# Kernel tuning notes

Hardware: AMD Instinct MI355X
Metric: run time of the kernel (lower is better)

The kernel has to match this reference:

```python
import jax, jax.numpy as jnp
import numpy as np

N = 20000      # num_nodes
E = 320000     # num_edges
T = 24         # seq_len
SD = 16        # static_dim
DD = 8         # dynamic_dim
HID = 128      # hidden_dim
HEADS = 4
DPH = HID // HEADS  # per-head dim (GATConv out_channels = hidden_dim // heads)
L = 3          # num_gnn_layers
LN_EPS = 1e-5


def setup_inputs() -> dict:
    key = jax.random.key(0)
    ks = jax.random.split(key, 16)
    f = lambda i, shape, s=0.1: jax.random.normal(ks[i], shape, jnp.float32) * s
    return {
        "x_static": f(0, (N, SD), 1.0),
        "x_dynamic": f(1, (T, N, DD), 1.0),
        "edge_index": jax.random.randint(ks[2], (2, E), 0, N),
        "proj_W": f(3, (SD + DD, HID)),
        "proj_b": jnp.zeros((HID,), jnp.float32),
        "gat_W": f(4, (L, HID, HID)),
        "att_src": f(5, (L, HEADS, DPH)),
        "att_dst": f(6, (L, HEADS, DPH)),
        "gat_b": jnp.zeros((L, HID), jnp.float32),
        "ln_g": jnp.ones((L, HID), jnp.float32),
        "ln_b": jnp.zeros((L, HID), jnp.float32),
        "lstm_Wih0": f(7, (4 * HID, HID)),
        "lstm_Whh0": f(8, (4 * HID, HID)),
        "lstm_bih0": jnp.zeros((4 * HID,), jnp.float32),
        "lstm_bhh0": jnp.zeros((4 * HID,), jnp.float32),
        "lstm_Wih1": f(9, (4 * HID, HID)),
        "lstm_Whh1": f(10, (4 * HID, HID)),
        "lstm_bih1": jnp.zeros((4 * HID,), jnp.float32),
        "lstm_bhh1": jnp.zeros((4 * HID,), jnp.float32),
        "out_W1": f(11, (HID, HID // 2)),
        "out_b1": jnp.zeros((HID // 2,), jnp.float32),
        "out_W2": f(12, (HID // 2, 1)),
        "out_b2": jnp.zeros((1,), jnp.float32),
    }


def _gat_layer(h, src, dst, W, a_s, a_d, b, g, beta):
    """PyG GATConv (self-loops already in src/dst) + residual + LayerNorm + ReLU."""
    Nn = h.shape[0]
    xp = (h @ W).reshape(Nn, HEADS, DPH)                # [N, H, D]
    a_src = (xp * a_s).sum(-1)                          # [N, H]
    a_dst = (xp * a_d).sum(-1)                          # [N, H]
    e = jax.nn.leaky_relu(a_src[src] + a_dst[dst], 0.2)  # [E', H]
    m = jax.ops.segment_max(e, dst, num_segments=Nn)
    ex = jnp.exp(e - m[dst])
    denom = jax.ops.segment_sum(ex, dst, num_segments=Nn)
    alpha = ex / (denom[dst] + 1e-16)                   # segment softmax over in-edges
    msg = xp[src] * alpha[:, :, None]                   # [E', H, D]
    out = jax.ops.segment_sum(msg, dst, num_segments=Nn).reshape(Nn, HID) + b
    out = out + h                                       # residual (dims match)
    mu = out.mean(-1, keepdims=True)
    var = ((out - mu) ** 2).mean(-1, keepdims=True)
    out = g * (out - mu) * jax.lax.rsqrt(var + LN_EPS) + beta
    return jax.nn.relu(out)


def _lstm_cell(x, h, c, Wih, Whh, bih, bhh):
    z = x @ Wih.T + h @ Whh.T + bih + bhh
    i, f, gg, o = jnp.split(z, 4, axis=-1)              # torch gate order i,f,g,o
    c = jax.nn.sigmoid(f) * c + jax.nn.sigmoid(i) * jnp.tanh(gg)
    h = jax.nn.sigmoid(o) * jnp.tanh(c)
    return h, c


def reference(x_static, x_dynamic, edge_index, proj_W, proj_b, gat_W, att_src,
              att_dst, gat_b, ln_g, ln_b, lstm_Wih0, lstm_Whh0, lstm_bih0,
              lstm_bhh0, lstm_Wih1, lstm_Whh1, lstm_bih1, lstm_bhh1,
              out_W1, out_b1, out_W2, out_b2):
    Nn = x_static.shape[0]
    loop = jnp.arange(Nn)
    src = jnp.concatenate([edge_index[0], loop])        # GATConv add_self_loops=True
    dst = jnp.concatenate([edge_index[1], loop])

    @jax.checkpoint
    def timestep(xd_t):
        h = jnp.concatenate([x_static, xd_t], axis=-1) @ proj_W + proj_b
        for l in range(L):
            h = _gat_layer(h, src, dst, gat_W[l], att_src[l], att_dst[l],
                           gat_b[l], ln_g[l], ln_b[l])
        return h

    h_seq = jax.lax.map(timestep, x_dynamic)            # [T, N, HID]

    def step(carry, x_t):
        h0, c0, h1, c1 = carry
        h0, c0 = _lstm_cell(x_t, h0, c0, lstm_Wih0, lstm_Whh0, lstm_bih0, lstm_bhh0)
        h1, c1 = _lstm_cell(h0, h1, c1, lstm_Wih1, lstm_Whh1, lstm_bih1, lstm_bhh1)
        return (h0, c0, h1, c1), None

    z = jnp.zeros((Nn, HID), x_static.dtype)
    (_, _, h1, _), _ = jax.lax.scan(step, (z, z, z, z), h_seq)
    pred = jax.nn.relu(h1 @ out_W1 + out_b1) @ out_W2 + out_b2
    return pred[:, 0]
```

## Files before the change

### kernel.cpp

```cpp
#include <hip/hip_runtime.h>
#include <hip/hip_bf16.h>
#include <math.h>

#define NN   20000
#define NE   320000
#define TT   24
#define SDIM 16
#define DDIM 8
#define HID  128
#define HEADS 4
#define DPH  32
#define NL   3
#define TC   4

typedef unsigned short u16;
typedef unsigned int   u32;
typedef __attribute__((ext_vector_type(8))) short  short8;
typedef __attribute__((ext_vector_type(4))) float  floatx4;

__device__ __forceinline__ u16 f2bf(float x) {
  u32 u = __float_as_uint(x);
  return (u16)((u + 0x7fff + ((u >> 16) & 1)) >> 16);
}
__device__ __forceinline__ float bf2f(u16 b) {
  return __uint_as_float(((u32)b) << 16);
}

__global__ void k_count(const int* __restrict__ dst, int* __restrict__ cnt) {
  int e = blockIdx.x * 256 + threadIdx.x;
  if (e < NE) atomicAdd(&cnt[dst[e]], 1);
}

__global__ __launch_bounds__(1024) void k_scan(const int* __restrict__ cnt,
    int* __restrict__ rowptr, int* __restrict__ cursor) {
  __shared__ int sh[1024];
  int tid = threadIdx.x;
  const int CH = 20;
  int base = tid * CH;
  int local[CH];
  int s = 0;
  #pragma unroll
  for (int i = 0; i < CH; i++) {
    int idx = base + i;
    int v = (idx < NN) ? cnt[idx] : 0;
    local[i] = s;
    s += v;
  }
  sh[tid] = s;
  __syncthreads();
  for (int off = 1; off < 1024; off <<= 1) {
    int tv = (tid >= off) ? sh[tid - off] : 0;
    __syncthreads();
    sh[tid] += tv;
    __syncthreads();
  }
  int pre = (tid > 0) ? sh[tid - 1] : 0;
  #pragma unroll
  for (int i = 0; i < CH; i++) {
    int idx = base + i;
    if (idx < NN) { int e = pre + local[i]; rowptr[idx] = e; cursor[idx] = e; }
  }
  if (tid == 1023) rowptr[NN] = sh[1023];
}

__global__ void k_fill(const int* __restrict__ src, const int* __restrict__ dst,
    int* __restrict__ cursor, int* __restrict__ col) {
  int e = blockIdx.x * 256 + threadIdx.x;
  if (e < NE) {
    int pos = atomicAdd(&cursor[dst[e]], 1);
    col[pos] = src[e];
  }
}

__global__ void k_prepw_lstm(const float* __restrict__ Wih, const float* __restrict__ Whh,
    u16* __restrict__ Bt) {
  int idx = blockIdx.x * 256 + threadIdx.x;
  if (idx < 512 * 256) {
    int jp = idx >> 8, k = idx & 255;
    int c = jp >> 2, g = jp & 3;
    int j = g * 128 + c;
    float v = (k < 128) ? Wih[(size_t)j * 128 + k] : Whh[(size_t)j * 128 + (k - 128)];
    Bt[idx] = f2bf(v);
  }
}
__global__ void k_prepb(const float* __restrict__ bih0, const float* __restrict__ bhh0,
    const float* __restrict__ bih1, const float* __restrict__ bhh1,
    float* __restrict__ bs01) {
  int t = threadIdx.x;
  const float* bih = blockIdx.x ? bih1 : bih0;
  const float* bhh = blockIdx.x ? bhh1 : bhh0;
  int c = t >> 2, g = t & 3;
  bs01[blockIdx.x * 512 + t] = bih[g * 128 + c] + bhh[g * 128 + c];
}
__global__ void k_prepw_gat(const float* __restrict__ gatW, u16* __restrict__ Btg) {
  int idx = blockIdx.x * 256 + threadIdx.x;
  if (idx < NL * 128 * 128) {
    int l = idx >> 14, r = idx & 16383;
    int n = r >> 7, k = r & 127;
    Btg[idx] = f2bf(gatW[(size_t)l * 16384 + k * 128 + n]);
  }
}

__global__ __launch_bounds__(256) void k_proj(const float* __restrict__ xs,
    const float* __restrict__ xdt, const float* __restrict__ W,
    const float* __restrict__ b, u16* __restrict__ hbf) {
  __shared__ float Ws[24 * HID];
  __shared__ float xin[16][24];
  int tid = threadIdx.x;
  int tc = blockIdx.y;
  for (int i = tid; i < 24 * HID; i += 256) Ws[i] = W[i];
  int n0 = blockIdx.x * 16;
  for (int i = tid; i < 16 * 24; i += 256) {
    int r = i / 24, c = i % 24;
    int n = n0 + r;
    xin[r][c] = (c < SDIM) ? xs[(size_t)n * SDIM + c]
                           : xdt[(size_t)tc * NN * DDIM + (size_t)n * DDIM + (c - SDIM)];
  }
  __syncthreads();
  int ch = tid & 127, rb = (tid >> 7) * 8;
  for (int r = rb; r < rb + 8; r++) {
    float acc = b[ch];
    #pragma unroll
    for (int k = 0; k < 24; k++) acc = fmaf(xin[r][k], Ws[k * HID + ch], acc);
    hbf[((size_t)tc * NN + n0 + r) * HID + ch] = f2bf(acc);
  }
}

#define TBM 128
#define TBN 64
#define TBK 64

__global__ __launch_bounds__(256) void k_bgemm_gat(const u16* __restrict__ A,
    const u16* __restrict__ Bt, const float* __restrict__ as_,
    const float* __restrict__ ad_, u16* __restrict__ xpbf,
    float* __restrict__ asrc, float* __restrict__ adst, int M) {
  __shared__ u16 As[TBM][TBK + 8];
  __shared__ u16 Bs[TBN][TBK + 8];
  int tid = threadIdx.x;
  int wid = tid >> 6, lane = tid & 63;
  int wr = wid >> 1, wc = wid & 1;
  int lrow = lane & 15, lgrp = lane >> 4;
  int row0 = blockIdx.x * TBM, col0 = blockIdx.y * TBN;
  floatx4 acc[4][2] = {};
  for (int k0 = 0; k0 < 128; k0 += TBK) {
    #pragma unroll
    for (int i = 0; i < 4; i++) {
      int idx = tid + i * 256;
      int r = idx >> 3, g = idx & 7;
      int gr = row0 + r;
      short8 v = {};
      if (gr < M) v = *(const short8*)(A + (size_t)gr * 128 + k0 + g * 8);
      *(short8*)&As[r][g * 8] = v;
    }
    #pragma unroll
    for (int i = 0; i < 2; i++) {
      int idx = tid + i * 256;
      int r = idx >> 3, g = idx & 7;
      *(short8*)&Bs[r][g * 8] = *(const short8*)(Bt + (size_t)(col0 + r) * 128 + k0 + g * 8);
    }
    __syncthreads();
    #pragma unroll
    for (int kk = 0; kk < TBK; kk += 32) {
      short8 bfr[2];
      #pragma unroll
      for (int n = 0; n < 2; n++)
        bfr[n] = *(const short8*)&Bs[wc * 32 + n * 16 + lrow][kk + lgrp * 8];
      #pragma unroll
      for (int m = 0; m < 4; m++) {
        short8 af = *(const short8*)&As[wr * 64 + m * 16 + lrow][kk + lgrp * 8];
        acc[m][0] = __builtin_amdgcn_mfma_f32_16x16x32_bf16(af, bfr[0], acc[m][0], 0, 0, 0);
        acc[m][1] = __builtin_amdgcn_mfma_f32_16x16x32_bf16(af, bfr[1], acc[m][1], 0, 0, 0);
      }
    }
    __syncthreads();
  }
  int head = (col0 >> 5) + wc;
  float as0 = as_[head * 32 + lrow], as1 = as_[head * 32 + 16 + lrow];
  float ad0 = ad_[head * 32 + lrow], ad1 = ad_[head * 32 + 16 + lrow];
  #pragma unroll
  for (int m = 0; m < 4; m++) {
    #pragma unroll
    for (int r = 0; r < 4; r++) {
      int grow = row0 + wr * 64 + m * 16 + lgrp * 4 + r;
      float v0 = acc[m][0][r], v1 = acc[m][1][r];
      if (grow < M) {
        xpbf[(size_t)grow * HID + col0 + wc * 32 + lrow]      = f2bf(v0);
        xpbf[(size_t)grow * HID + col0 + wc * 32 + 16 + lrow] = f2bf(v1);
      }
      float ps = v0 * as0 + v1 * as1;
      float pd = v0 * ad0 + v1 * ad1;
      #pragma unroll
      for (int off = 1; off < 16; off <<= 1) {
        ps += __shfl_xor(ps, off);
        pd += __shfl_xor(pd, off);
      }
      if (lrow == 0 && grow < M) {
        asrc[grow * HEADS + head] = ps;
        adst[grow * HEADS + head] = pd;
      }
    }
  }
}

__global__ __launch_bounds__(256) void k_aggr(const u16* __restrict__ xpbf,
    u16* __restrict__ hbf, const float* __restrict__ asrc,
    const float* __restrict__ adst, const int* __restrict__ rowptr,
    const int* __restrict__ col, const float* __restrict__ bias,
    const float* __restrict__ lng, const float* __restrict__ lnb) {
  int wid = threadIdx.x >> 6, lane = threadIdx.x & 63;
  int n = blockIdx.x * 4 + wid;
  int tc = n / NN;
  int node = n - tc * NN, base = tc * NN;
  int hh = lane >> 4;
  float ad = adst[n * HEADS + hh];
  float e0 = asrc[n * HEADS + hh] + ad;
  e0 = (e0 > 0.f) ? e0 : 0.2f * e0;
  float w0 = __expf(fminf(e0, 80.f));
  u32 xv = ((const u32*)(xpbf + (size_t)n * HID))[lane];
  float den0 = w0, den1 = 0.f, den2 = 0.f, den3 = 0.f;
  float p00 = w0 * bf2f((u16)(xv & 0xffff)), p10 = 0.f, p20 = 0.f, p30 = 0.f;
  float p01 = w0 * bf2f((u16)(xv >> 16)),    p11 = 0.f, p21 = 0.f, p31 = 0.f;
  int rs = rowptr[node], re = rowptr[node + 1];
  int j = rs;
  for (; j + 4 <= re; j += 4) {
    int s0 = base + col[j],     s1 = base + col[j + 1];
    int s2 = base + col[j + 2], s3 = base + col[j + 3];
    float ev0 = asrc[s0 * HEADS + hh] + ad;
    float ev1 = asrc[s1 * HEADS + hh] + ad;
    float ev2 = asrc[s2 * HEADS + hh] + ad;
    float ev3 = asrc[s3 * HEADS + hh] + ad;
    u32 x0 = ((const u32*)(xpbf + (size_t)s0 * HID))[lane];
    u32 x1 = ((const u32*)(xpbf + (size_t)s1 * HID))[lane];
    u32 x2 = ((const u32*)(xpbf + (size_t)s2 * HID))[lane];
    u32 x3 = ((const u32*)(xpbf + (size_t)s3 * HID))[lane];
    ev0 = (ev0 > 0.f) ? ev0 : 0.2f * ev0;
    ev1 = (ev1 > 0.f) ? ev1 : 0.2f * ev1;
    ev2 = (ev2 > 0.f) ? ev2 : 0.2f * ev2;
    ev3 = (ev3 > 0.f) ? ev3 : 0.2f * ev3;
    float w0e = __expf(fminf(ev0, 80.f));
    float w1e = __expf(fminf(ev1, 80.f));
    float w2e = __expf(fminf(ev2, 80.f));
    float w3e = __expf(fminf(ev3, 80.f));
    den0 += w0e; den1 += w1e; den2 += w2e; den3 += w3e;
    p00 = fmaf(w0e, bf2f((u16)(x0 & 0xffff)), p00);
    p10 = fmaf(w1e, bf2f((u16)(x1 & 0xffff)), p10);
    p20 = fmaf(w2e, bf2f((u16)(x2 & 0xffff)), p20);
    p30 = fmaf(w3e, bf2f((u16)(x3 & 0xffff)), p30);
    p01 = fmaf(w0e, bf2f((u16)(x0 >> 16)), p01);
    p11 = fmaf(w1e, bf2f((u16)(x1 >> 16)), p11);
    p21 = fmaf(w2e, bf2f((u16)(x2 >> 16)), p21);
    p31 = fmaf(w3e, bf2f((u16)(x3 >> 16)), p31);
  }
  for (; j < re; j++) {
    int s0 = base + col[j];
    float ev = asrc[s0 * HEADS + hh] + ad;
    ev = (ev > 0.f) ? ev : 0.2f * ev;
    u32 x0 = ((const u32*)(xpbf + (size_t)s0 * HID))[lane];
    float w = __expf(fminf(ev, 80.f));
    den0 += w;
    p00 = fmaf(w, bf2f((u16)(x0 & 0xffff)), p00);
    p01 = fmaf(w, bf2f((u16)(x0 >> 16)), p01);
  }
  float den = (den0 + den1) + (den2 + den3);
  float mg0 = (p00 + p10) + (p20 + p30);
  float mg1 = (p01 + p11) + (p21 + p31);
  float inv = 1.f / (den + 1e-16f);
  int c0 = lane * 2;
  size_t hoff = (size_t)n * HID + c0;
  u32 hv = *(const u32*)(hbf + hoff);
  float o0 = mg0 * inv + bias[c0]     + bf2f((u16)(hv & 0xffff));
  float o1 = mg1 * inv + bias[c0 + 1] + bf2f((u16)(hv >> 16));
  float s2 = o0 + o1;
  #pragma unroll
  for (int off = 32; off; off >>= 1) s2 += __shfl_xor(s2, off);
  float mu = s2 * (1.f / HID);
  float d0 = o0 - mu, d1 = o1 - mu;
  float v2 = d0 * d0 + d1 * d1;
  #pragma unroll
  for (int off = 32; off; off >>= 1) v2 += __shfl_xor(v2, off);
  float rstd = rsqrtf(v2 * (1.f / HID) + 1e-5f);
  o0 = lng[c0] * d0 * rstd + lnb[c0];
  o1 = lng[c0 + 1] * d1 * rstd + lnb[c0 + 1];
  o0 = fmaxf(o0, 0.f);
  o1 = fmaxf(o1, 0.f);
  *(u32*)(hbf + hoff) = (u32)f2bf(o0) | ((u32)f2bf(o1) << 16);
}

__global__ __launch_bounds__(256) void k_bgemm_lstm(const u16* __restrict__ A0,
    const u16* __restrict__ A1, const u16* __restrict__ Bt,
    const float* __restrict__ bs, float* __restrict__ cst,
    u16* __restrict__ hout, int M) {
  __shared__ __align__(16) char smem[34816];
  u16 (*As)[TBK + 8] = (u16(*)[TBK + 8])smem;
  u16 (*Bs)[TBK + 8] = (u16(*)[TBK + 8])(smem + TBM * (TBK + 8) * 2);
  float (*zs)[68] = (float(*)[68])smem;
  int tid = threadIdx.x;
  int wid = tid >> 6, lane = tid & 63;
  int wr = wid >> 1, wc = wid & 1;
  int lrow = lane & 15, lgrp = lane >> 4;
  int row0 = blockIdx.x * TBM, col0 = blockIdx.y * TBN;
  floatx4 acc[4][2] = {};
  for (int k0 = 0; k0 < 256; k0 += TBK) {
    const u16* Ap = (k0 < 128) ? A0 : A1;
    int kb = k0 & 127;
    #pragma unroll
    for (int i = 0; i < 4; i++) {
      int idx = tid + i * 256;
      int r = idx >> 3, g = idx & 7;
      int gr = row0 + r;
      short8 v = {};
      if (gr < M) v = *(const short8*)(Ap + (size_t)gr * 128 + kb + g * 8);
      *(short8*)&As[r][g * 8] = v;
    }
    #pragma unroll
    for (int i = 0; i < 2; i++) {
      int idx = tid + i * 256;
      int r = idx >> 3, g = idx & 7;
      *(short8*)&Bs[r][g * 8] = *(const short8*)(Bt + (size_t)(col0 + r) * 256 + k0 + g * 8);
    }
    __syncthreads();
    #pragma unroll
    for (int kk = 0; kk < TBK; kk += 32) {
      short8 bfr[2];
      #pragma unroll
      for (int n = 0; n < 2; n++)
        bfr[n] = *(const short8*)&Bs[wc * 32 + n * 16 + lrow][kk + lgrp * 8];
      #pragma unroll
      for (int m = 0; m < 4; m++) {
        short8 af = *(const short8*)&As[wr * 64 + m * 16 + lrow][kk + lgrp * 8];
        acc[m][0] = __builtin_amdgcn_mfma_f32_16x16x32_bf16(af, bfr[0], acc[m][0], 0, 0, 0);
        acc[m][1] = __builtin_amdgcn_mfma_f32_16x16x32_bf16(af, bfr[1], acc[m][1], 0, 0, 0);
      }
    }
    __syncthreads();
  }
  #pragma unroll
  for (int m = 0; m < 4; m++)
    #pragma unroll
    for (int n = 0; n < 2; n++)
      #pragma unroll
      for (int r = 0; r < 4; r++)
        zs[wr * 64 + m * 16 + lgrp * 4 + r][wc * 32 + n * 16 + lrow] = acc[m][n][r];
  __syncthreads();
  int ch0 = blockIdx.y * 16;
  #pragma unroll
  for (int it = 0; it < 8; it++) {
    int o = tid + it * 256;
    int r = o >> 4, lc = o & 15;
    int grow = row0 + r;
    if (grow < M) {
      float4 zi = *(float4*)&zs[r][lc * 4];
      int ch = ch0 + lc;
      size_t gi = (size_t)grow * HID + ch;
      float ii = zi.x + bs[4 * ch + 0];
      float ff = zi.y + bs[4 * ch + 1];
      float gg = zi.z + bs[4 * ch + 2];
      float oo = zi.w + bs[4 * ch + 3];
      float si = 1.f / (1.f + __expf(-ii));
      float sf = 1.f / (1.f + __expf(-ff));
      float so = 1.f / (1.f + __expf(-oo));
      float tg = tanhf(gg);
      float cn = sf * cst[gi] + si * tg;
      cst[gi] = cn;
      hout[gi] = f2bf(so * tanhf(cn));
    }
  }
}

__global__ __launch_bounds__(64) void k_mlp(const u16* __restrict__ h1,
    const float* __restrict__ W1, const float* __restrict__ b1,
    const float* __restrict__ W2, const float* __restrict__ b2,
    float* __restrict__ out) {
  int n = blockIdx.x, j = threadIdx.x;
  const u16* hr = h1 + (size_t)n * HID;
  float acc = b1[j];
  #pragma unroll 8
  for (int k = 0; k < HID; k++) acc = fmaf(bf2f(hr[k]), W1[(size_t)k * 64 + j], acc);
  acc = fmaxf(acc, 0.f);
  float p = acc * W2[j];
  #pragma unroll
  for (int off = 32; off; off >>= 1) p += __shfl_xor(p, off);
  if (j == 0) out[n] = p + b2[0];
}

extern "C" void kernel_launch(void* const* d_in, const int* in_sizes, int n_in,
                              void* d_out, int out_size, void* d_ws, size_t ws_size,
                              hipStream_t stream) {
  const float* xs    = (const float*)d_in[0];
  const float* xd    = (const float*)d_in[1];
  const int*   ei    = (const int*)d_in[2];
  const float* projW = (const float*)d_in[3];
  const float* projb = (const float*)d_in[4];
  const float* gatW  = (const float*)d_in[5];
  const float* attS  = (const float*)d_in[6];
  const float* attD  = (const float*)d_in[7];
  const float* gatb  = (const float*)d_in[8];
  const float* lng   = (const float*)d_in[9];
  const float* lnb   = (const float*)d_in[10];
  const float* Wih0  = (const float*)d_in[11];
  const float* Whh0  = (const float*)d_in[12];
  const float* bih0  = (const float*)d_in[13];
  const float* bhh0  = (const float*)d_in[14];
  const float* Wih1  = (const float*)d_in[15];
  const float* Whh1  = (const float*)d_in[16];
  const float* bih1  = (const float*)d_in[17];
  const float* bhh1  = (const float*)d_in[18];
  const float* oW1   = (const float*)d_in[19];
  const float* ob1   = (const float*)d_in[20];
  const float* oW2   = (const float*)d_in[21];
  const float* ob2   = (const float*)d_in[22];
  float* out = (float*)d_out;

  char* w = (char*)d_ws;
  size_t off = 0;
  auto alloc = [&](size_t bytes) { void* p = w + off; off += (bytes + 255) & ~(size_t)255; return p; };
  u16*   hbf   = (u16*)  alloc((size_t)TC * NN * HID * 2);
  u16*   xpbf  = (u16*)  alloc((size_t)TC * NN * HID * 2);
  float* asrc  = (float*)alloc((size_t)TC * NN * HEADS * 4);
  float* adst  = (float*)alloc((size_t)TC * NN * HEADS * 4);
  float* c01   = (float*)alloc((size_t)2 * NN * HID * 4);
  float* c0 = c01, *c1 = c01 + (size_t)NN * HID;
  u16*   h0p   = (u16*)  alloc((size_t)2 * NN * HID * 2);
  u16*   h1p   = (u16*)  alloc((size_t)2 * NN * HID * 2);
  u16*   h0buf[2] = { h0p, h0p + (size_t)NN * HID };
  u16*   h1buf[2] = { h1p, h1p + (size_t)NN * HID };
  u16*   Wc0bf = (u16*)alloc((size_t)512 * 256 * 2);
  u16*   Wc1bf = (u16*)alloc((size_t)512 * 256 * 2);
  float* bs01  = (float*)alloc((size_t)1024 * 4);
  float* bs0 = bs01, *bs1 = bs01 + 512;
  u16*   gatWbf= (u16*)alloc((size_t)NL * 128 * 128 * 2);
  int* cnt    = (int*)alloc((size_t)NN * 4);
  int* rowptr = (int*)alloc((size_t)(NN + 1) * 4);
  int* cursor = (int*)alloc((size_t)NN * 4);
  int* col    = (int*)alloc((size_t)NE * 4);

  const int* esrc = ei;
  const int* edst = ei + NE;

  hipMemsetAsync(cnt, 0, (size_t)NN * 4, stream);
  k_count<<<(NE + 255) / 256, 256, 0, stream>>>(edst, cnt);
  k_scan<<<1, 1024, 0, stream>>>(cnt, rowptr, cursor);
  k_fill<<<(NE + 255) / 256, 256, 0, stream>>>(esrc, edst, cursor, col);

  k_prepw_lstm<<<(512 * 256) / 256, 256, 0, stream>>>(Wih0, Whh0, Wc0bf);
  k_prepw_lstm<<<(512 * 256) / 256, 256, 0, stream>>>(Wih1, Whh1, Wc1bf);
  k_prepb<<<2, 512, 0, stream>>>(bih0, bhh0, bih1, bhh1, bs01);
  k_prepw_gat<<<(NL * 128 * 128) / 256, 256, 0, stream>>>(gatW, gatWbf);
  hipMemsetAsync(c01, 0, (size_t)2 * NN * HID * 4, stream);
  hipMemsetAsync(h0buf[0], 0, (size_t)NN * HID * 2, stream);
  hipMemsetAsync(h1buf[0], 0, (size_t)NN * HID * 2, stream);

  const int gx  = (NN + TBM - 1) / TBM;
  const int gx2 = (TC * NN + TBM - 1) / TBM;
  for (int tcb = 0; tcb < TT / TC; tcb++) {
    k_proj<<<dim3(NN / 16, TC), 256, 0, stream>>>(
        xs, xd + (size_t)(tcb * TC) * NN * DDIM, projW, projb, hbf);
    for (int l = 0; l < NL; l++) {
      k_bgemm_gat<<<dim3(gx2, 2), 256, 0, stream>>>(
          hbf, gatWbf + (size_t)l * 128 * 128,
          attS + l * HEADS * DPH, attD + l * HEADS * DPH,
          xpbf, asrc, adst, TC * NN);
      k_aggr<<<TC * NN / 4, 256, 0, stream>>>(
          xpbf, hbf, asrc, adst, rowptr, col, gatb + (size_t)l * HID,
          lng + (size_t)l * HID, lnb + (size_t)l * HID);
    }
    for (int s2 = 0; s2 < TC; s2++) {
      int t = tcb * TC + s2;
      int pi = t & 1;
      k_bgemm_lstm<<<dim3(gx, 8), 256, 0, stream>>>(
          hbf + (size_t)s2 * NN * HID, h0buf[pi], Wc0bf, bs0, c0, h0buf[pi ^ 1], NN);
      k_bgemm_lstm<<<dim3(gx, 8), 256, 0, stream>>>(
          h0buf[pi ^ 1], h1buf[pi], Wc1bf, bs1, c1, h1buf[pi ^ 1], NN);
    }
  }

  k_mlp<<<NN, 64, 0, stream>>>(h1buf[0], oW1, ob1, oW2, ob2, out);
}
```

Baseline: 3.499 ms.

## Precompute GAT edge weights and fuse skewed LSTM layer steps into one launch

Measured after the change: 3.318 ms. -5.2%, faster.

```diff
diff --git a/kernel.cpp b/kernel.cpp
--- a/kernel.cpp
+++ b/kernel.cpp
@@ -64,11 +64,13 @@
 }
 
 __global__ void k_fill(const int* __restrict__ src, const int* __restrict__ dst,
-    int* __restrict__ cursor, int* __restrict__ col) {
+    int* __restrict__ cursor, int* __restrict__ col, int* __restrict__ row) {
   int e = blockIdx.x * 256 + threadIdx.x;
   if (e < NE) {
-    int pos = atomicAdd(&cursor[dst[e]], 1);
+    int d = dst[e];
+    int pos = atomicAdd(&cursor[d], 1);
     col[pos] = src[e];
+    row[pos] = d;
   }
 }
 
@@ -202,11 +204,27 @@
   }
 }
 
+__global__ __launch_bounds__(256) void k_edgew(const int* __restrict__ col,
+    const int* __restrict__ row, const float* __restrict__ asrc,
+    const float* __restrict__ adst, float* __restrict__ wbuf) {
+  int idx = blockIdx.x * 256 + threadIdx.x;
+  int h = idx & 3;
+  int je = idx >> 2;
+  int tc = je / NE;
+  int j = je - tc * NE;
+  int base = tc * NN;
+  float ev = asrc[(size_t)(base + col[j]) * HEADS + h]
+           + adst[(size_t)(base + row[j]) * HEADS + h];
+  ev = (ev > 0.f) ? ev : 0.2f * ev;
+  wbuf[idx] = __expf(fminf(ev, 80.f));
+}
+
 __global__ __launch_bounds__(256) void k_aggr(const u16* __restrict__ xpbf,
     u16* __restrict__ hbf, const float* __restrict__ asrc,
-    const float* __restrict__ adst, const int* __restrict__ rowptr,
-    const int* __restrict__ col, const float* __restrict__ bias,
-    const float* __restrict__ lng, const float* __restrict__ lnb) {
+    const float* __restrict__ adst, const float* __restrict__ wbuf,
+    const int* __restrict__ rowptr, const int* __restrict__ col,
+    const float* __restrict__ bias, const float* __restrict__ lng,
+    const float* __restrict__ lnb) {
   int wid = threadIdx.x >> 6, lane = threadIdx.x & 63;
   int n = blockIdx.x * 4 + wid;
   int tc = n / NN;
@@ -220,27 +238,20 @@
   float den0 = w0, den1 = 0.f, den2 = 0.f, den3 = 0.f;
   float p00 = w0 * bf2f((u16)(xv & 0xffff)), p10 = 0.f, p20 = 0.f, p30 = 0.f;
   float p01 = w0 * bf2f((u16)(xv >> 16)),    p11 = 0.f, p21 = 0.f, p31 = 0.f;
+  const float* wrow = wbuf + (size_t)tc * NE * HEADS;
   int rs = rowptr[node], re = rowptr[node + 1];
   int j = rs;
   for (; j + 4 <= re; j += 4) {
+    float w0e = wrow[(size_t)(j + 0) * HEADS + hh];
+    float w1e = wrow[(size_t)(j + 1) * HEADS + hh];
+    float w2e = wrow[(size_t)(j + 2) * HEADS + hh];
+    float w3e = wrow[(size_t)(j + 3) * HEADS + hh];
     int s0 = base + col[j],     s1 = base + col[j + 1];
     int s2 = base + col[j + 2], s3 = base + col[j + 3];
-    float ev0 = asrc[s0 * HEADS + hh] + ad;
-    float ev1 = asrc[s1 * HEADS + hh] + ad;
-    float ev2 = asrc[s2 * HEADS + hh] + ad;
-    float ev3 = asrc[s3 * HEADS + hh] + ad;
     u32 x0 = ((const u32*)(xpbf + (size_t)s0 * HID))[lane];
     u32 x1 = ((const u32*)(xpbf + (size_t)s1 * HID))[lane];
     u32 x2 = ((const u32*)(xpbf + (size_t)s2 * HID))[lane];
     u32 x3 = ((const u32*)(xpbf + (size_t)s3 * HID))[lane];
-    ev0 = (ev0 > 0.f) ? ev0 : 0.2f * ev0;
-    ev1 = (ev1 > 0.f) ? ev1 : 0.2f * ev1;
-    ev2 = (ev2 > 0.f) ? ev2 : 0.2f * ev2;
-    ev3 = (ev3 > 0.f) ? ev3 : 0.2f * ev3;
-    float w0e = __expf(fminf(ev0, 80.f));
-    float w1e = __expf(fminf(ev1, 80.f));
-    float w2e = __expf(fminf(ev2, 80.f));
-    float w3e = __expf(fminf(ev3, 80.f));
     den0 += w0e; den1 += w1e; den2 += w2e; den3 += w3e;
     p00 = fmaf(w0e, bf2f((u16)(x0 & 0xffff)), p00);
     p10 = fmaf(w1e, bf2f((u16)(x1 & 0xffff)), p10);
@@ -252,11 +263,9 @@
     p31 = fmaf(w3e, bf2f((u16)(x3 >> 16)), p31);
   }
   for (; j < re; j++) {
+    float w = wrow[(size_t)j * HEADS + hh];
     int s0 = base + col[j];
-    float ev = asrc[s0 * HEADS + hh] + ad;
-    ev = (ev > 0.f) ? ev : 0.2f * ev;
     u32 x0 = ((const u32*)(xpbf + (size_t)s0 * HID))[lane];
-    float w = __expf(fminf(ev, 80.f));
     den0 += w;
     p00 = fmaf(w, bf2f((u16)(x0 & 0xffff)), p00);
     p01 = fmaf(w, bf2f((u16)(x0 >> 16)), p01);
@@ -286,11 +295,10 @@
   *(u32*)(hbf + hoff) = (u32)f2bf(o0) | ((u32)f2bf(o1) << 16);
 }
 
-__global__ __launch_bounds__(256) void k_bgemm_lstm(const u16* __restrict__ A0,
+__device__ __forceinline__ void lstm_body(const u16* __restrict__ A0,
     const u16* __restrict__ A1, const u16* __restrict__ Bt,
     const float* __restrict__ bs, float* __restrict__ cst,
-    u16* __restrict__ hout, int M) {
-  __shared__ __align__(16) char smem[34816];
+    u16* __restrict__ hout, char* smem, int bx, int by) {
   u16 (*As)[TBK + 8] = (u16(*)[TBK + 8])smem;
   u16 (*Bs)[TBK + 8] = (u16(*)[TBK + 8])(smem + TBM * (TBK + 8) * 2);
   float (*zs)[68] = (float(*)[68])smem;
@@ -298,7 +306,7 @@
   int wid = tid >> 6, lane = tid & 63;
   int wr = wid >> 1, wc = wid & 1;
   int lrow = lane & 15, lgrp = lane >> 4;
-  int row0 = blockIdx.x * TBM, col0 = blockIdx.y * TBN;
+  int row0 = bx * TBM, col0 = by * TBN;
   floatx4 acc[4][2] = {};
   for (int k0 = 0; k0 < 256; k0 += TBK) {
     const u16* Ap = (k0 < 128) ? A0 : A1;
@@ -309,7 +317,7 @@
       int r = idx >> 3, g = idx & 7;
       int gr = row0 + r;
       short8 v = {};
-      if (gr < M) v = *(const short8*)(Ap + (size_t)gr * 128 + kb + g * 8);
+      if (gr < NN) v = *(const short8*)(Ap + (size_t)gr * 128 + kb + g * 8);
       *(short8*)&As[r][g * 8] = v;
     }
     #pragma unroll
@@ -342,13 +350,13 @@
       for (int r = 0; r < 4; r++)
         zs[wr * 64 + m * 16 + lgrp * 4 + r][wc * 32 + n * 16 + lrow] = acc[m][n][r];
   __syncthreads();
-  int ch0 = blockIdx.y * 16;
+  int ch0 = by * 16;
   #pragma unroll
   for (int it = 0; it < 8; it++) {
     int o = tid + it * 256;
     int r = o >> 4, lc = o & 15;
     int grow = row0 + r;
-    if (grow < M) {
+    if (grow < NN) {
       float4 zi = *(float4*)&zs[r][lc * 4];
       int ch = ch0 + lc;
       size_t gi = (size_t)grow * HID + ch;
@@ -365,6 +373,23 @@
       hout[gi] = f2bf(so * tanhf(cn));
     }
   }
+}
+
+__global__ __launch_bounds__(256) void k_lstm1(const u16* __restrict__ A0,
+    const u16* __restrict__ A1, const u16* __restrict__ Bt,
+    const float* __restrict__ bs, float* __restrict__ cst, u16* __restrict__ hout) {
+  __shared__ __align__(16) char smem[34816];
+  lstm_body(A0, A1, Bt, bs, cst, hout, smem, blockIdx.x, blockIdx.y);
+}
+
+__global__ __launch_bounds__(256) void k_lstm2(
+    const u16* __restrict__ A0a, const u16* __restrict__ A1a, const u16* __restrict__ Bta,
+    const float* __restrict__ bsa, float* __restrict__ csta, u16* __restrict__ houta,
+    const u16* __restrict__ A0b, const u16* __restrict__ A1b, const u16* __restrict__ Btb,
+    const float* __restrict__ bsb, float* __restrict__ cstb, u16* __restrict__ houtb) {
+  __shared__ __align__(16) char smem[34816];
+  if (blockIdx.z == 0) lstm_body(A0a, A1a, Bta, bsa, csta, houta, smem, blockIdx.x, blockIdx.y);
+  else                 lstm_body(A0b, A1b, Btb, bsb, cstb, houtb, smem, blockIdx.x, blockIdx.y);
 }
 
 __global__ __launch_bounds__(64) void k_mlp(const u16* __restrict__ h1,
@@ -418,6 +443,7 @@
   u16*   xpbf  = (u16*)  alloc((size_t)TC * NN * HID * 2);
   float* asrc  = (float*)alloc((size_t)TC * NN * HEADS * 4);
   float* adst  = (float*)alloc((size_t)TC * NN * HEADS * 4);
+  float* wbuf  = (float*)alloc((size_t)TC * NE * HEADS * 4);
   float* c01   = (float*)alloc((size_t)2 * NN * HID * 4);
   float* c0 = c01, *c1 = c01 + (size_t)NN * HID;
   u16*   h0p   = (u16*)  alloc((size_t)2 * NN * HID * 2);
@@ -433,6 +459,7 @@
   int* rowptr = (int*)alloc((size_t)(NN + 1) * 4);
   int* cursor = (int*)alloc((size_t)NN * 4);
   int* col    = (int*)alloc((size_t)NE * 4);
+  int* rowi   = (int*)alloc((size_t)NE * 4);
 
   const int* esrc = ei;
   const int* edst = ei + NE;
@@ -440,7 +467,7 @@
   hipMemsetAsync(cnt, 0, (size_t)NN * 4, stream);
   k_count<<<(NE + 255) / 256, 256, 0, stream>>>(edst, cnt);
   k_scan<<<1, 1024, 0, stream>>>(cnt, rowptr, cursor);
-  k_fill<<<(NE + 255) / 256, 256, 0, stream>>>(esrc, edst, cursor, col);
+  k_fill<<<(NE + 255) / 256, 256, 0, stream>>>(esrc, edst, cursor, col, rowi);
 
   k_prepw_lstm<<<(512 * 256) / 256, 256, 0, stream>>>(Wih0, Whh0, Wc0bf);
   k_prepw_lstm<<<(512 * 256) / 256, 256, 0, stream>>>(Wih1, Whh1, Wc1bf);
@@ -452,7 +479,8 @@
 
   const int gx  = (NN + TBM - 1) / TBM;
   const int gx2 = (TC * NN + TBM - 1) / TBM;
-  for (int tcb = 0; tcb < TT / TC; tcb++) {
+
+  auto gnn_chunk = [&](int tcb) {
     k_proj<<<dim3(NN / 16, TC), 256, 0, stream>>>(
         xs, xd + (size_t)(tcb * TC) * NN * DDIM, projW, projb, hbf);
     for (int l = 0; l < NL; l++) {
@@ -460,17 +488,32 @@
           hbf, gatWbf + (size_t)l * 128 * 128,
           attS + l * HEADS * DPH, attD + l * HEADS * DPH,
           xpbf, asrc, adst, TC * NN);
+      k_edgew<<<(TC * NE * HEADS) / 256, 256, 0, stream>>>(col, rowi, asrc, adst, wbuf);
       k_aggr<<<TC * NN / 4, 256, 0, stream>>>(
-          xpbf, hbf, asrc, adst, rowptr, col, gatb + (size_t)l * HID,
+          xpbf, hbf, asrc, adst, wbuf, rowptr, col, gatb + (size_t)l * HID,
           lng + (size_t)l * HID, lnb + (size_t)l * HID);
     }
-    for (int s2 = 0; s2 < TC; s2++) {
-      int t = tcb * TC + s2;
-      int pi = t & 1;
-      k_bgemm_lstm<<<dim3(gx, 8), 256, 0, stream>>>(
-          hbf + (size_t)s2 * NN * HID, h0buf[pi], Wc0bf, bs0, c0, h0buf[pi ^ 1], NN);
-      k_bgemm_lstm<<<dim3(gx, 8), 256, 0, stream>>>(
-          h0buf[pi ^ 1], h1buf[pi], Wc1bf, bs1, c1, h1buf[pi ^ 1], NN);
+  };
+  auto lstm_merged = [&](int t) {
+    int pi = t & 1;
+    int s1 = (t + 1) & (TC - 1);
+    k_lstm2<<<dim3(gx, 8, 2), 256, 0, stream>>>(
+        h0buf[pi ^ 1], h1buf[pi], Wc1bf, bs1, c1, h1buf[pi ^ 1],
+        hbf + (size_t)s1 * NN * HID, h0buf[pi ^ 1], Wc0bf, bs0, c0, h0buf[pi]);
+  };
+
+  gnn_chunk(0);
+  k_lstm1<<<dim3(gx, 8), 256, 0, stream>>>(hbf, h0buf[0], Wc0bf, bs0, c0, h0buf[1]);
+  lstm_merged(0); lstm_merged(1); lstm_merged(2);
+  for (int tcb = 1; tcb < TT / TC; tcb++) {
+    gnn_chunk(tcb);
+    lstm_merged(4 * tcb - 1);
+    lstm_merged(4 * tcb);
+    lstm_merged(4 * tcb + 1);
+    if (tcb < TT / TC - 1) lstm_merged(4 * tcb + 2);
+    else {
+      lstm_merged(4 * tcb + 2);
+      k_lstm1<<<dim3(gx, 8), 256, 0, stream>>>(h0buf[0], h1buf[1], Wc1bf, bs1, c1, h1buf[0]);
     }
   }
 
```
